# Kernel optimization log

Measured on AMD Instinct MI355X. Metric: run time of the kernel, lower is better.

Reference implementation:

```python
import jax, jax.numpy as jnp
import numpy as np

N, D_IN, D_H, D_OUT, E = 65536, 512, 1024, 512, 8


def setup_inputs() -> dict:
    key = jax.random.key(0)
    ks = jax.random.split(key, 9)
    s_in = 1.0 / np.sqrt(D_IN)
    s_h = 1.0 / np.sqrt(D_H)
    x = jax.random.normal(ks[0], (N, D_IN), dtype=jnp.float32)
    Wg = jax.random.uniform(ks[1], (D_IN, E), minval=-s_in, maxval=s_in, dtype=jnp.float32)
    bg = jax.random.uniform(ks[2], (E,), minval=-s_in, maxval=s_in, dtype=jnp.float32)
    # stacked per-expert MLP params: Linear(d_in->h), ReLU, Linear(h->h), ReLU, Linear(h->d_out)
    W0 = jax.random.uniform(ks[3], (E, D_IN, D_H), minval=-s_in, maxval=s_in, dtype=jnp.float32)
    b0 = jax.random.uniform(ks[4], (E, D_H), minval=-s_in, maxval=s_in, dtype=jnp.float32)
    W1 = jax.random.uniform(ks[5], (E, D_H, D_H), minval=-s_h, maxval=s_h, dtype=jnp.float32)
    b1 = jax.random.uniform(ks[6], (E, D_H), minval=-s_h, maxval=s_h, dtype=jnp.float32)
    W2 = jax.random.uniform(ks[7], (E, D_H, D_OUT), minval=-s_h, maxval=s_h, dtype=jnp.float32)
    b2 = jax.random.uniform(ks[8], (E, D_OUT), minval=-s_h, maxval=s_h, dtype=jnp.float32)
    return {"x": x, "Wg": Wg, "bg": bg, "W0": W0, "b0": b0, "W1": W1, "b1": b1, "W2": W2, "b2": b2}


def reference(x, Wg, bg, W0, b0, W1, b1, W2, b2):
    # Gating (eval path): hard argmax one-hot; selected weight is exactly 1.0
    logits = x @ Wg + bg                       # [N, E]
    idx = jnp.argmax(logits, axis=-1)          # [N]
    onehot = jax.nn.one_hot(idx, E, dtype=x.dtype)  # [N, E]
    out = jnp.zeros((x.shape[0], D_OUT), dtype=x.dtype)
    # loop over small fixed expert count; tokens fully vectorized
    for e in range(E):
        h = jax.nn.relu(x @ W0[e] + b0[e])     # [N, h]
        h = jax.nn.relu(h @ W1[e] + b1[e])     # [N, h]
        y = h @ W2[e] + b2[e]                  # [N, d_out]
        out = out + y * onehot[:, e:e + 1]
    return out
```

## Files before the change

kernel.cpp:

```cpp
#include <hip/hip_runtime.h>
#include <stdint.h>

#define N_TOK 65536
#define DIN   512
#define DH    1024
#define DOUT  512
#define NE    8
#define MP_CAP 66560
#define ROW_BLOCKS 520
#define CSTRIDE 144

typedef __bf16 bf16x8 __attribute__((ext_vector_type(8)));
typedef float  f32x4  __attribute__((ext_vector_type(4)));

typedef __attribute__((address_space(3))) void  lds_void;
typedef const __attribute__((address_space(1))) void g_void;

__device__ __forceinline__ float bf2f(unsigned short u) {
  union { unsigned int i; float f; } v; v.i = ((unsigned int)u) << 16; return v.f;
}
__device__ __forceinline__ unsigned short f2bf(float f) {
  unsigned int u = __builtin_bit_cast(unsigned int, f);
  u += 0x7fffu + ((u >> 16) & 1u);
  return (unsigned short)(u >> 16);
}

__global__ void detect_k(const unsigned short* __restrict__ x, int* __restrict__ flag) {
  __shared__ int cnt;
  if (threadIdx.x == 0) cnt = 0;
  __syncthreads();
  int c = 0;
  for (int i = threadIdx.x; i < 16384; i += 256) {
    const unsigned short u = x[2 * i];
    const int ex = (u >> 7) & 0xFF;
    if (ex > 140) ++c;
  }
  atomicAdd(&cnt, c);
  __syncthreads();
  if (threadIdx.x == 0) flag[0] = (cnt > 512) ? 1 : 0;
}

__global__ __launch_bounds__(256)
void conv_x_k(const void* __restrict__ xin, unsigned short* __restrict__ xc,
              const int* __restrict__ flag) {
  if (!flag[0]) return;
  const int i = (blockIdx.x * 256 + threadIdx.x) * 8;
  const float* xf = (const float*)xin;
  unsigned short o[8];
#pragma unroll
  for (int j = 0; j < 8; ++j) o[j] = f2bf(xf[i + j]);
  *(uint4*)&xc[i] = *(const uint4*)o;
}

__global__ void conv_bias_k(const void* __restrict__ b, float* __restrict__ out, int n,
                            const int* __restrict__ flag) {
  const int i = blockIdx.x * 256 + threadIdx.x;
  if (i < n) out[i] = flag[0] ? ((const float*)b)[i] : bf2f(((const unsigned short*)b)[i]);
}

__global__ __launch_bounds__(1024)
void transpose_k(const void* __restrict__ W, unsigned short* __restrict__ WT,
                 int K, int Nn, const int* __restrict__ flag) {
  __shared__ unsigned short tile[64][65];
  const int fv = flag[0];
  const int e = blockIdx.z;
  const size_t base = (size_t)e * K * Nn;
  unsigned short* dst = WT + base;
  const int n0 = blockIdx.x * 64, k0 = blockIdx.y * 64;
  const int tx = threadIdx.x, ty = threadIdx.y;
#pragma unroll
  for (int i = 0; i < 4; ++i) {
    const size_t idx = base + (size_t)(k0 + ty + i * 16) * Nn + n0 + tx;
    tile[ty + i * 16][tx] = fv ? f2bf(((const float*)W)[idx])
                               : ((const unsigned short*)W)[idx];
  }
  __syncthreads();
#pragma unroll
  for (int i = 0; i < 4; ++i)
    dst[(size_t)(n0 + ty + i * 16) * K + k0 + tx] = tile[tx][ty + i * 16];
}

__global__ __launch_bounds__(256)
void gating_k(const void* __restrict__ x, const void* __restrict__ Wg,
              const void* __restrict__ bg, int* __restrict__ eidx,
              const int* __restrict__ flag) {
  const int wv = threadIdx.x >> 6, lane = threadIdx.x & 63;
  const int t = blockIdx.x * 4 + wv;
  const int fv = flag[0];
  double acc[8];
#pragma unroll
  for (int e = 0; e < 8; ++e) acc[e] = 0.0;
  if (fv) {
    const float* xr = (const float*)x + (size_t)t * DIN;
    const float* wg = (const float*)Wg;
#pragma unroll
    for (int i = 0; i < 8; ++i) {
      const int k = i * 64 + lane;
      const double xv = (double)xr[k];
#pragma unroll
      for (int e = 0; e < 8; ++e) acc[e] += xv * (double)wg[(size_t)k * 8 + e];
    }
  } else {
    const unsigned short* xr = (const unsigned short*)x + (size_t)t * DIN;
    const unsigned short* wg = (const unsigned short*)Wg;
#pragma unroll
    for (int i = 0; i < 8; ++i) {
      const int k = i * 64 + lane;
      const double xv = (double)bf2f(xr[k]);
      const uint4 wq = *(const uint4*)(wg + (size_t)k * 8);
      acc[0] += xv * (double)bf2f((unsigned short)(wq.x & 0xffff));
      acc[1] += xv * (double)bf2f((unsigned short)(wq.x >> 16));
      acc[2] += xv * (double)bf2f((unsigned short)(wq.y & 0xffff));
      acc[3] += xv * (double)bf2f((unsigned short)(wq.y >> 16));
      acc[4] += xv * (double)bf2f((unsigned short)(wq.z & 0xffff));
      acc[5] += xv * (double)bf2f((unsigned short)(wq.z >> 16));
      acc[6] += xv * (double)bf2f((unsigned short)(wq.w & 0xffff));
      acc[7] += xv * (double)bf2f((unsigned short)(wq.w >> 16));
    }
  }
#pragma unroll
  for (int o = 32; o > 0; o >>= 1)
#pragma unroll
    for (int e = 0; e < 8; ++e) acc[e] += __shfl_down(acc[e], o, 64);
  if (lane == 0) {
    int bi = 0;
    double best = acc[0] + (double)(fv ? ((const float*)bg)[0]
                                       : bf2f(((const unsigned short*)bg)[0]));
#pragma unroll
    for (int e = 1; e < 8; ++e) {
      const double v = acc[e] + (double)(fv ? ((const float*)bg)[e]
                                            : bf2f(((const unsigned short*)bg)[e]));
      if (v > best) { best = v; bi = e; }
    }
    eidx[t] = bi;
  }
}

__global__ __launch_bounds__(256)
void count_k(const int* __restrict__ eidx, int* __restrict__ counts) {
  __shared__ int h[8];
  if (threadIdx.x < 8) h[threadIdx.x] = 0;
  __syncthreads();
  atomicAdd(&h[eidx[blockIdx.x * 256 + threadIdx.x]], 1);
  __syncthreads();
  if (threadIdx.x < 8) atomicAdd(&counts[threadIdx.x], h[threadIdx.x]);
}

__global__ void offsets_k(const int* __restrict__ counts, int* __restrict__ off,
                          int* __restrict__ fill) {
  if (threadIdx.x == 0) {
    int a = 0;
    off[0] = 0;
    for (int e = 0; e < 8; ++e) {
      a += (counts[e] + 127) & ~127;
      off[e + 1] = a;
    }
  }
  if (threadIdx.x < 8) fill[threadIdx.x] = 0;
}

__global__ __launch_bounds__(256)
void scatter_k(const int* __restrict__ eidx, const int* __restrict__ off,
               int* __restrict__ fill, int* __restrict__ rowmap) {
  const int t = blockIdx.x * 256 + threadIdx.x;
  const int lane = threadIdx.x & 63;
  const int e = eidx[t];
#pragma unroll
  for (int ex = 0; ex < 8; ++ex) {
    unsigned long long m = __ballot(e == ex);
    if (e == ex) {
      const unsigned long long lt = (1ULL << lane) - 1ULL;
      const int rank = __popcll(m & lt);
      const int leader = __ffsll((unsigned long long)m) - 1;
      int base = 0;
      if (lane == leader) base = atomicAdd(&fill[ex], (int)__popcll(m));
      base = __shfl(base, leader, 64);
      rowmap[off[ex] + base + rank] = t;
    }
  }
}

template <int GATHER, int RELU, int SCATTER>
__global__ __launch_bounds__(256, 2)
void gemm_k(const unsigned short* __restrict__ A, const unsigned short* __restrict__ Axc,
            const unsigned short* __restrict__ BT,
            const float* __restrict__ biasF, void* __restrict__ C,
            const int* __restrict__ rowmap, const int* __restrict__ off,
            const int* __restrict__ flag, const int K, const int Nc, const int rowBase,
            const int ncb, const int lncb) {
  __shared__ __align__(16) unsigned short smem[128 * CSTRIDE];
  unsigned short* As = smem;
  unsigned short* Bs = smem + 128 * 64;

  const int segBlocksLocal = gridDim.x >> lncb;
  const int fullRows = segBlocksLocal & ~7;
  const int fullBlocks = fullRows << lncb;
  int col, rowg;
  {
    const int p = blockIdx.x;
    if (p < fullBlocks) {
      const int xcd = p & 7, qq = p >> 3;
      col = qq & (ncb - 1);
      rowg = ((qq >> lncb) << 3) + xcd;
    } else {
      const int r = p - fullBlocks;
      col = r & (ncb - 1);
      rowg = fullRows + (r >> lncb);
    }
  }

  const int Mp = off[8];
  const int rowStart = rowBase + rowg * 128;
  if (rowStart >= Mp) return;
  int e = 0;
#pragma unroll
  for (int j = 1; j <= 8; ++j) e += (off[j] <= rowStart) ? 1 : 0;

  const int colStart = col * 128;
  const int tid = threadIdx.x;
  const int w = tid >> 6, lane = tid & 63;
  const int subrow = lane >> 3;
  const int q = lane & 7;
  const int slot = q ^ subrow;

  const unsigned short* Ause = (GATHER && flag[0]) ? Axc : A;
  const unsigned short* Be = BT + (size_t)e * Nc * K;

  const unsigned short* aptr[4];
  const unsigned short* bptr[4];
  int ldsOff[4];
#pragma unroll
  for (int i = 0; i < 4; ++i) {
    const int r = i * 32 + w * 8 + subrow;
    int arow;
    if (GATHER) {
      arow = rowmap[rowStart + r];
      if (arow < 0) arow = 0;
    } else {
      arow = rowStart + r - rowBase;
    }
    aptr[i] = Ause + (size_t)arow * K + slot * 8;
    bptr[i] = Be + (size_t)(colStart + r) * K + slot * 8;
    ldsOff[i] = (i * 32 + w * 8) * 64;
  }

  const int wm = w >> 1, wn = w & 1;
  const int fr = lane & 15, quad = lane >> 4;

  f32x4 acc[4][4];
#pragma unroll
  for (int i = 0; i < 4; ++i)
#pragma unroll
    for (int j = 0; j < 4; ++j) acc[i][j] = (f32x4){0.f, 0.f, 0.f, 0.f};

  int aoff[2][4], boff[2][4];
#pragma unroll
  for (int s = 0; s < 2; ++s)
#pragma unroll
    for (int i = 0; i < 4; ++i) {
      const int qq = quad + s * 4;
      const int rowA = wm * 64 + i * 16 + fr;
      aoff[s][i] = rowA * 64 + (qq ^ (rowA & 7)) * 8;
      const int rowB = wn * 64 + i * 16 + fr;
      boff[s][i] = rowB * 64 + (qq ^ (rowB & 7)) * 8;
    }

  for (int k0 = 0; k0 < K; k0 += 64) {
#pragma unroll
    for (int i = 0; i < 4; ++i) {
      __builtin_amdgcn_global_load_lds((g_void*)(aptr[i] + k0),
                                       (lds_void*)(As + ldsOff[i]), 16, 0, 0);
      __builtin_amdgcn_global_load_lds((g_void*)(bptr[i] + k0),
                                       (lds_void*)(Bs + ldsOff[i]), 16, 0, 0);
    }
    __syncthreads();
    bf16x8 af[2][4], bfv[2][4];
#pragma unroll
    for (int s = 0; s < 2; ++s)
#pragma unroll
      for (int i = 0; i < 4; ++i) {
        af[s][i] = *(const bf16x8*)&As[aoff[s][i]];
        bfv[s][i] = *(const bf16x8*)&Bs[boff[s][i]];
      }
#pragma unroll
    for (int s = 0; s < 2; ++s)
#pragma unroll
      for (int i = 0; i < 4; ++i)
#pragma unroll
        for (int j = 0; j < 4; ++j)
          acc[i][j] = __builtin_amdgcn_mfma_f32_16x16x32_bf16(af[s][i], bfv[s][j],
                                                              acc[i][j], 0, 0, 0);
    __syncthreads();
  }

  const int flagv = SCATTER ? flag[0] : 0;
  float bv2[4];
#pragma unroll
  for (int j = 0; j < 4; ++j)
    bv2[j] = biasF[(size_t)e * Nc + colStart + wn * 64 + j * 16 + fr];

  if (SCATTER && flagv) {
#pragma unroll
    for (int i = 0; i < 4; ++i)
#pragma unroll
      for (int r = 0; r < 4; ++r) {
        const int gr = rowStart + wm * 64 + i * 16 + quad * 4 + r;
        const int crow = rowmap[gr];
        if (crow < 0) continue;
        const size_t cbase = (size_t)crow * Nc + colStart + wn * 64 + fr;
#pragma unroll
        for (int j = 0; j < 4; ++j)
          ((float*)C)[cbase + j * 16] = acc[i][j][r] + bv2[j];
      }
    return;
  }

#pragma unroll
  for (int i = 0; i < 4; ++i)
#pragma unroll
    for (int r = 0; r < 4; ++r) {
      const int row = wm * 64 + i * 16 + quad * 4 + r;
#pragma unroll
      for (int j = 0; j < 4; ++j) {
        float v = acc[i][j][r] + bv2[j];
        if (RELU) v = fmaxf(v, 0.f);
        smem[row * CSTRIDE + wn * 64 + j * 16 + fr] = f2bf(v);
      }
    }
  __syncthreads();

#pragma unroll
  for (int it = 0; it < 8; ++it) {
    const int idx = it * 256 + tid;
    const int row = idx >> 4, c16 = idx & 15;
    int crow;
    if (SCATTER) {
      crow = rowmap[rowStart + row];
      if (crow < 0) continue;
    } else {
      crow = rowStart + row - rowBase;
    }
    const uint4 vv = *(const uint4*)&smem[row * CSTRIDE + c16 * 8];
    *(uint4*)&((unsigned short*)C)[(size_t)crow * Nc + colStart + c16 * 8] = vv;
  }
}

extern "C" void kernel_launch(void* const* d_in, const int* in_sizes, int n_in,
                              void* d_out, int out_size, void* d_ws, size_t ws_size,
                              hipStream_t stream) {
  const void* x  = d_in[0];
  const void* Wg = d_in[1];
  const void* bg = d_in[2];
  const void* W0 = d_in[3];
  const void* b0 = d_in[4];
  const void* W1 = d_in[5];
  const void* b1 = d_in[6];
  const void* W2 = d_in[7];
  const void* b2 = d_in[8];

  char* ws = (char*)d_ws;
  unsigned short* WT0 = (unsigned short*)(ws + 0);
  unsigned short* WT1 = (unsigned short*)(ws + 8388608);
  unsigned short* WT2 = (unsigned short*)(ws + 25165824);
  unsigned short* xc  = (unsigned short*)(ws + 33554432);
  float* bf0 = (float*)(ws + 100663296);
  float* bf1 = (float*)(ws + 100696064);
  float* bf2 = (float*)(ws + 100728832);
  int* rowmap = (int*)(ws + 100745216);
  int* eidx   = (int*)(ws + 101011456);
  int* counts = (int*)(ws + 101273600);
  int* off    = (int*)(ws + 101273664);
  int* fill   = (int*)(ws + 101273728);
  int* flag   = (int*)(ws + 101273792);
  const size_t FIXED = 101274624;
  unsigned short* h0 = (unsigned short*)(ws + FIXED);

  int segBlocks = 1;
  if (ws_size > FIXED + 524288) {
    size_t sb = (ws_size - FIXED) / 524288;
    segBlocks = (sb > ROW_BLOCKS) ? ROW_BLOCKS : (int)sb;
    if (segBlocks >= 8) segBlocks &= ~7;
  }
  unsigned short* h1 = h0 + (size_t)segBlocks * 128 * DH;
  const int nseg = (ROW_BLOCKS + segBlocks - 1) / segBlocks;

  hipMemsetAsync(counts, 0, 8 * sizeof(int), stream);
  hipMemsetAsync(rowmap, 0xFF, MP_CAP * sizeof(int), stream);

  detect_k<<<1, 256, 0, stream>>>((const unsigned short*)x, flag);

  conv_x_k<<<N_TOK * DIN / 8 / 256, 256, 0, stream>>>(x, xc, flag);
  conv_bias_k<<<(NE * DH + 255) / 256, 256, 0, stream>>>(b0, bf0, NE * DH, flag);
  conv_bias_k<<<(NE * DH + 255) / 256, 256, 0, stream>>>(b1, bf1, NE * DH, flag);
  conv_bias_k<<<(NE * DOUT + 255) / 256, 256, 0, stream>>>(b2, bf2, NE * DOUT, flag);

  transpose_k<<<dim3(DH / 64, DIN / 64, NE), dim3(64, 16), 0, stream>>>(W0, WT0, DIN, DH, flag);
  transpose_k<<<dim3(DH / 64, DH / 64, NE), dim3(64, 16), 0, stream>>>(W1, WT1, DH, DH, flag);
  transpose_k<<<dim3(DOUT / 64, DH / 64, NE), dim3(64, 16), 0, stream>>>(W2, WT2, DH, DOUT, flag);

  gating_k<<<N_TOK / 4, 256, 0, stream>>>(x, Wg, bg, eidx, flag);
  count_k<<<N_TOK / 256, 256, 0, stream>>>(eidx, counts);
  offsets_k<<<1, 64, 0, stream>>>(counts, off, fill);
  scatter_k<<<N_TOK / 256, 256, 0, stream>>>(eidx, off, fill, rowmap);

  for (int s = 0; s < nseg; ++s) {
    const int rowBase = s * segBlocks * 128;
    gemm_k<1, 1, 0><<<dim3(8 * segBlocks), 256, 0, stream>>>(
        (const unsigned short*)x, xc, WT0, bf0, h0, rowmap, off, flag, DIN, DH, rowBase, 8, 3);
    gemm_k<0, 1, 0><<<dim3(8 * segBlocks), 256, 0, stream>>>(
        h0, h0, WT1, bf1, h1, rowmap, off, flag, DH, DH, rowBase, 8, 3);
    gemm_k<0, 0, 1><<<dim3(4 * segBlocks), 256, 0, stream>>>(
        h1, h1, WT2, bf2, d_out, rowmap, off, flag, DH, DOUT, rowBase, 4, 2);
  }
}
```

Baseline: 862.9 us.

## Fuse preprocessing kernels and merge x conversion into gating pass

Collapses the memsets, bias conversions, three transposes, count and offset kernels into fewer launches. The x-to-bf16 conversion moves into the gating kernel, so x is read once for both gating and conversion. The gating weights are staged transposed in LDS, and each block builds a local histogram. Offsets are recomputed per thread inside scatter. A __syncthreads is also added before the epilogue's shared-memory staging. This reduces launch overhead and one full pass over x, at the cost of each gating block reloading Wg into LDS (16384 blocks of 16KB).

```diff
diff --git a/kernel.cpp b/kernel.cpp
--- a/kernel.cpp
+++ b/kernel.cpp
@@ -25,8 +25,10 @@
   return (unsigned short)(u >> 16);
 }
 
-__global__ void detect_k(const unsigned short* __restrict__ x, int* __restrict__ flag) {
+__global__ void detect_k(const unsigned short* __restrict__ x, int* __restrict__ flag,
+                         int* __restrict__ counts, int* __restrict__ fill) {
   __shared__ int cnt;
+  if (threadIdx.x < 8) { counts[threadIdx.x] = 0; fill[threadIdx.x] = 0; }
   if (threadIdx.x == 0) cnt = 0;
   __syncthreads();
   int c = 0;
@@ -41,33 +43,47 @@
 }
 
 __global__ __launch_bounds__(256)
-void conv_x_k(const void* __restrict__ xin, unsigned short* __restrict__ xc,
-              const int* __restrict__ flag) {
-  if (!flag[0]) return;
-  const int i = (blockIdx.x * 256 + threadIdx.x) * 8;
-  const float* xf = (const float*)xin;
-  unsigned short o[8];
-#pragma unroll
-  for (int j = 0; j < 8; ++j) o[j] = f2bf(xf[i + j]);
-  *(uint4*)&xc[i] = *(const uint4*)o;
-}
-
-__global__ void conv_bias_k(const void* __restrict__ b, float* __restrict__ out, int n,
-                            const int* __restrict__ flag) {
-  const int i = blockIdx.x * 256 + threadIdx.x;
-  if (i < n) out[i] = flag[0] ? ((const float*)b)[i] : bf2f(((const unsigned short*)b)[i]);
+void prep_k(const void* __restrict__ b0, const void* __restrict__ b1,
+            const void* __restrict__ b2, float* __restrict__ bf0,
+            float* __restrict__ bf1, float* __restrict__ bf2,
+            int* __restrict__ rowmap, const int* __restrict__ flag) {
+  const int b = blockIdx.x;
+  if (b < 65) {
+    const int i = (b * 256 + threadIdx.x) * 4;
+    *(int4*)&rowmap[i] = (int4){-1, -1, -1, -1};
+    return;
+  }
+  const int fv = flag[0];
+  const int i = (b - 65) * 256 + threadIdx.x;
+  const void* src; float* dst; int li;
+  if (i < NE * DH) { src = b0; dst = bf0; li = i; }
+  else if (i < 2 * NE * DH) { src = b1; dst = bf1; li = i - NE * DH; }
+  else { src = b2; dst = bf2; li = i - 2 * NE * DH; }
+  dst[li] = fv ? ((const float*)src)[li] : bf2f(((const unsigned short*)src)[li]);
 }
 
 __global__ __launch_bounds__(1024)
-void transpose_k(const void* __restrict__ W, unsigned short* __restrict__ WT,
-                 int K, int Nn, const int* __restrict__ flag) {
+void transpose_all_k(const void* __restrict__ W0, const void* __restrict__ W1,
+                     const void* __restrict__ W2, unsigned short* __restrict__ WT0,
+                     unsigned short* __restrict__ WT1, unsigned short* __restrict__ WT2,
+                     const int* __restrict__ flag) {
   __shared__ unsigned short tile[64][65];
   const int fv = flag[0];
-  const int e = blockIdx.z;
+  int b = blockIdx.x;
+  const void* W; unsigned short* WT; int K, Nn, e, n0, k0;
+  if (b < 1024) {
+    W = W0; WT = WT0; K = DIN; Nn = DH;
+    e = b >> 7; const int r = b & 127; n0 = (r & 15) * 64; k0 = (r >> 4) * 64;
+  } else if (b < 3072) {
+    b -= 1024; W = W1; WT = WT1; K = DH; Nn = DH;
+    e = b >> 8; const int r = b & 255; n0 = (r & 15) * 64; k0 = (r >> 4) * 64;
+  } else {
+    b -= 3072; W = W2; WT = WT2; K = DH; Nn = DOUT;
+    e = b >> 7; const int r = b & 127; n0 = (r & 7) * 64; k0 = (r >> 3) * 64;
+  }
   const size_t base = (size_t)e * K * Nn;
   unsigned short* dst = WT + base;
-  const int n0 = blockIdx.x * 64, k0 = blockIdx.y * 64;
-  const int tx = threadIdx.x, ty = threadIdx.y;
+  const int tx = threadIdx.x & 63, ty = threadIdx.x >> 6;
 #pragma unroll
   for (int i = 0; i < 4; ++i) {
     const size_t idx = base + (size_t)(k0 + ty + i * 16) * Nn + n0 + tx;
@@ -81,41 +97,59 @@
 }
 
 __global__ __launch_bounds__(256)
-void gating_k(const void* __restrict__ x, const void* __restrict__ Wg,
-              const void* __restrict__ bg, int* __restrict__ eidx,
-              const int* __restrict__ flag) {
-  const int wv = threadIdx.x >> 6, lane = threadIdx.x & 63;
+void gating_fused_k(const void* __restrict__ x, const void* __restrict__ Wg,
+                    const void* __restrict__ bg, unsigned short* __restrict__ xc,
+                    int* __restrict__ eidx, int* __restrict__ counts,
+                    const int* __restrict__ flag) {
+  __shared__ float wgT[NE * DIN];
+  __shared__ int hist[8];
+  const int tid = threadIdx.x;
+  const int fv = flag[0];
+  if (tid < 8) hist[tid] = 0;
+  if (fv) {
+    const float* wg = (const float*)Wg;
+    for (int idx = tid; idx < NE * DIN; idx += 256) {
+      const int k = idx >> 3, e = idx & 7;
+      wgT[e * DIN + k] = wg[idx];
+    }
+  } else {
+    const unsigned short* wg = (const unsigned short*)Wg;
+    for (int idx = tid; idx < NE * DIN; idx += 256) {
+      const int k = idx >> 3, e = idx & 7;
+      wgT[e * DIN + k] = bf2f(wg[idx]);
+    }
+  }
+  __syncthreads();
+
+  const int wv = tid >> 6, lane = tid & 63;
   const int t = blockIdx.x * 4 + wv;
-  const int fv = flag[0];
   double acc[8];
 #pragma unroll
   for (int e = 0; e < 8; ++e) acc[e] = 0.0;
+
   if (fv) {
     const float* xr = (const float*)x + (size_t)t * DIN;
-    const float* wg = (const float*)Wg;
+    float xs[8];
 #pragma unroll
     for (int i = 0; i < 8; ++i) {
       const int k = i * 64 + lane;
-      const double xv = (double)xr[k];
-#pragma unroll
-      for (int e = 0; e < 8; ++e) acc[e] += xv * (double)wg[(size_t)k * 8 + e];
-    }
+      const float xf = xr[k];
+      xs[i] = xf;
+      const double xv = (double)xf;
+#pragma unroll
+      for (int e = 0; e < 8; ++e) acc[e] += xv * (double)wgT[e * DIN + k];
+    }
+    unsigned short* xo = xc + (size_t)t * DIN;
+#pragma unroll
+    for (int i = 0; i < 8; ++i) xo[i * 64 + lane] = f2bf(xs[i]);
   } else {
     const unsigned short* xr = (const unsigned short*)x + (size_t)t * DIN;
-    const unsigned short* wg = (const unsigned short*)Wg;
 #pragma unroll
     for (int i = 0; i < 8; ++i) {
       const int k = i * 64 + lane;
       const double xv = (double)bf2f(xr[k]);
-      const uint4 wq = *(const uint4*)(wg + (size_t)k * 8);
-      acc[0] += xv * (double)bf2f((unsigned short)(wq.x & 0xffff));
-      acc[1] += xv * (double)bf2f((unsigned short)(wq.x >> 16));
-      acc[2] += xv * (double)bf2f((unsigned short)(wq.y & 0xffff));
-      acc[3] += xv * (double)bf2f((unsigned short)(wq.y >> 16));
-      acc[4] += xv * (double)bf2f((unsigned short)(wq.z & 0xffff));
-      acc[5] += xv * (double)bf2f((unsigned short)(wq.z >> 16));
-      acc[6] += xv * (double)bf2f((unsigned short)(wq.w & 0xffff));
-      acc[7] += xv * (double)bf2f((unsigned short)(wq.w >> 16));
+#pragma unroll
+      for (int e = 0; e < 8; ++e) acc[e] += xv * (double)wgT[e * DIN + k];
     }
   }
 #pragma unroll
@@ -133,35 +167,28 @@
       if (v > best) { best = v; bi = e; }
     }
     eidx[t] = bi;
-  }
+    atomicAdd(&hist[bi], 1);
+  }
+  __syncthreads();
+  if (tid < 8 && hist[tid]) atomicAdd(&counts[tid], hist[tid]);
 }
 
 __global__ __launch_bounds__(256)
-void count_k(const int* __restrict__ eidx, int* __restrict__ counts) {
-  __shared__ int h[8];
-  if (threadIdx.x < 8) h[threadIdx.x] = 0;
-  __syncthreads();
-  atomicAdd(&h[eidx[blockIdx.x * 256 + threadIdx.x]], 1);
-  __syncthreads();
-  if (threadIdx.x < 8) atomicAdd(&counts[threadIdx.x], h[threadIdx.x]);
-}
-
-__global__ void offsets_k(const int* __restrict__ counts, int* __restrict__ off,
-                          int* __restrict__ fill) {
-  if (threadIdx.x == 0) {
+void scatter_k(const int* __restrict__ eidx, const int* __restrict__ counts,
+               int* __restrict__ off_g, int* __restrict__ fill,
+               int* __restrict__ rowmap) {
+  int off[8];
+  {
     int a = 0;
-    off[0] = 0;
-    for (int e = 0; e < 8; ++e) {
-      a += (counts[e] + 127) & ~127;
-      off[e + 1] = a;
-    }
-  }
-  if (threadIdx.x < 8) fill[threadIdx.x] = 0;
-}
-
-__global__ __launch_bounds__(256)
-void scatter_k(const int* __restrict__ eidx, const int* __restrict__ off,
-               int* __restrict__ fill, int* __restrict__ rowmap) {
+#pragma unroll
+    for (int e2 = 0; e2 < 8; ++e2) { off[e2] = a; a += (counts[e2] + 127) & ~127; }
+    if (blockIdx.x == 0 && threadIdx.x == 0) {
+      off_g[0] = 0;
+      int aa = 0;
+#pragma unroll
+      for (int e2 = 0; e2 < 8; ++e2) { aa += (counts[e2] + 127) & ~127; off_g[e2 + 1] = aa; }
+    }
+  }
   const int t = blockIdx.x * 256 + threadIdx.x;
   const int lane = threadIdx.x & 63;
   const int e = eidx[t];
@@ -315,6 +342,7 @@
     return;
   }
 
+  __syncthreads();
 #pragma unroll
   for (int i = 0; i < 4; ++i)
 #pragma unroll
@@ -384,24 +412,16 @@
   unsigned short* h1 = h0 + (size_t)segBlocks * 128 * DH;
   const int nseg = (ROW_BLOCKS + segBlocks - 1) / segBlocks;
 
-  hipMemsetAsync(counts, 0, 8 * sizeof(int), stream);
-  hipMemsetAsync(rowmap, 0xFF, MP_CAP * sizeof(int), stream);
-
-  detect_k<<<1, 256, 0, stream>>>((const unsigned short*)x, flag);
-
-  conv_x_k<<<N_TOK * DIN / 8 / 256, 256, 0, stream>>>(x, xc, flag);
-  conv_bias_k<<<(NE * DH + 255) / 256, 256, 0, stream>>>(b0, bf0, NE * DH, flag);
-  conv_bias_k<<<(NE * DH + 255) / 256, 256, 0, stream>>>(b1, bf1, NE * DH, flag);
-  conv_bias_k<<<(NE * DOUT + 255) / 256, 256, 0, stream>>>(b2, bf2, NE * DOUT, flag);
-
-  transpose_k<<<dim3(DH / 64, DIN / 64, NE), dim3(64, 16), 0, stream>>>(W0, WT0, DIN, DH, flag);
-  transpose_k<<<dim3(DH / 64, DH / 64, NE), dim3(64, 16), 0, stream>>>(W1, WT1, DH, DH, flag);
-  transpose_k<<<dim3(DOUT / 64, DH / 64, NE), dim3(64, 16), 0, stream>>>(W2, WT2, DH, DOUT, flag);
-
-  gating_k<<<N_TOK / 4, 256, 0, stream>>>(x, Wg, bg, eidx, flag);
-  count_k<<<N_TOK / 256, 256, 0, stream>>>(eidx, counts);
-  offsets_k<<<1, 64, 0, stream>>>(counts, off, fill);
-  scatter_k<<<N_TOK / 256, 256, 0, stream>>>(eidx, off, fill, rowmap);
+  detect_k<<<1, 256, 0, stream>>>((const unsigned short*)x, flag, counts, fill);
+
+  prep_k<<<65 + (3 * NE * DH - NE * DH + NE * DOUT + NE * DH + 255) / 256, 256, 0, stream>>>(
+      b0, b1, b2, bf0, bf1, bf2, rowmap, flag);
+
+  transpose_all_k<<<4096, 1024, 0, stream>>>(W0, W1, W2, WT0, WT1, WT2, flag);
+
+  gating_fused_k<<<N_TOK / 4, 256, 0, stream>>>(x, Wg, bg, xc, eidx, counts, flag);
+
+  scatter_k<<<N_TOK / 256, 256, 0, stream>>>(eidx, counts, off, fill, rowmap);
 
   for (int s = 0; s < nseg; ++s) {
     const int rowBase = s * segBlocks * 128;
```

Result: slower. 918.3 us (+6.4%).
